# Optimization experiments

Measured on AMD Instinct MI355X. Metric: run time of the kernel, lower is better.

Reference implementation:

```python
import jax, jax.numpy as jnp
import numpy as np

D = 768       # input_dim / model width
H = 3072      # expert hidden width (init arg 'output_dim')
E = 8         # num_experts
K = 2         # top_k
NOISE_STD = 0.1
B, S = 2, 1024


def setup_inputs() -> dict:
    key = jax.random.key(0)
    ks = jax.random.split(key, 16)
    sd = lambda fan_in: 1.0 / np.sqrt(fan_in)
    return {
        "x": jax.random.normal(ks[0], (B, S, D), dtype=jnp.float32),
        "noise": jax.random.normal(ks[1], (B, S, E), dtype=jnp.float32),
        # router
        "Wr": jax.random.normal(ks[2], (D, E), dtype=jnp.float32) * sd(D),
        "br": jnp.zeros((E,), dtype=jnp.float32),
        # stacked expert FFNs: d -> h -> d
        "W1": jax.random.normal(ks[3], (E, D, H), dtype=jnp.float32) * sd(D),
        "b1": jnp.zeros((E, H), dtype=jnp.float32),
        "W2": jax.random.normal(ks[4], (E, H, D), dtype=jnp.float32) * sd(H),
        "b2": jnp.zeros((E, D), dtype=jnp.float32),
        # shared expert
        "Ws1": jax.random.normal(ks[5], (D, H), dtype=jnp.float32) * sd(D),
        "bs1": jnp.zeros((H,), dtype=jnp.float32),
        "Ws2": jax.random.normal(ks[6], (H, D), dtype=jnp.float32) * sd(H),
        "bs2": jnp.zeros((D,), dtype=jnp.float32),
        # mixing scalars (alpha trainable, beta frozen in torch)
        "alpha": jnp.float32(0.3),
        "beta": jnp.float32(0.7),
    }


def reference(x, noise, Wr, br, W1, b1, W2, b2, Ws1, bs1, Ws2, bs2, alpha, beta):
    b, s, d = x.shape
    xt = x.reshape(-1, d)                       # [T, D]
    nt = noise.reshape(-1, E)                   # [T, E]
    T = xt.shape[0]

    # router: noisy logits -> top-k -> softmax over selected experts only
    logits = xt @ Wr + br + NOISE_STD * nt      # [T, E]
    top_vals, top_idx = jax.lax.top_k(logits, K)  # [T, K]
    top_w = jax.nn.softmax(top_vals, axis=-1)     # softmax over -inf-masked logits == softmax over top-k
    gates = jnp.zeros((T, E), dtype=x.dtype).at[jnp.arange(T)[:, None], top_idx].set(top_w)  # [T, E], 0 elsewhere

    # experts (dense over E; non-selected contributions are zeroed by gates)
    h = jax.nn.leaky_relu(jnp.einsum('td,edh->teh', xt, W1) + b1, negative_slope=0.01)  # [T, E, H]
    y = jnp.einsum('teh,ehd->ted', h, W2) + b2                                          # [T, E, D]
    moe_out = jnp.einsum('ted,te->td', y, gates)                                        # [T, D]

    # shared expert
    sh = jax.nn.leaky_relu(xt @ Ws1 + bs1, negative_slope=0.01)
    shared_out = sh @ Ws2 + bs2                                                         # [T, D]

    w = jax.nn.softmax(jnp.stack([alpha, beta]))
    out = shared_out * w[0] + moe_out * w[1]
    return out.reshape(b, s, d)
```

## Files before the change

kernel.cpp:

```cpp
#include <hip/hip_runtime.h>
#include <hip/hip_bf16.h>
#include <cstdio>
#include <cstdint>

#define TNUM 2048
#define DDIM 768
#define HDIM 3072
#define ENUM 8

#define WAITVM(N) asm volatile("s_waitcnt vmcnt(" #N ")" ::: "memory")
#define MEMFENCE() asm volatile("" ::: "memory")

typedef __attribute__((ext_vector_type(8))) __bf16 bf16x8;
typedef __attribute__((ext_vector_type(4))) float f32x4;
typedef __attribute__((ext_vector_type(8))) unsigned short ushort8_t;

__device__ __forceinline__ unsigned short f2bf(float f) {
    __bf16 h = (__bf16)f;
    unsigned short u;
    __builtin_memcpy(&u, &h, 2);
    return u;
}

__device__ __forceinline__ void async_cp16(const unsigned short* g, unsigned short* l) {
    __builtin_amdgcn_global_load_lds((const __attribute__((address_space(1))) void*)g,
                                     (__attribute__((address_space(3))) void*)l,
                                     16, 0, 0);
}

__global__ void cast_x_kernel(const float* __restrict__ x, unsigned short* __restrict__ xb) {
    int i = (blockIdx.x * 256 + threadIdx.x) * 8;
    float4 a = *(const float4*)(x + i);
    float4 b = *(const float4*)(x + i + 4);
    ushort4 lo = make_ushort4(f2bf(a.x), f2bf(a.y), f2bf(a.z), f2bf(a.w));
    ushort4 hi = make_ushort4(f2bf(b.x), f2bf(b.y), f2bf(b.z), f2bf(b.w));
    *(ushort4*)(xb + i) = lo;
    *(ushort4*)(xb + i + 4) = hi;
}

__global__ __launch_bounds__(256)
void transw_kernel(const float* __restrict__ W1, const float* __restrict__ W2,
                   const float* __restrict__ Ws1, const float* __restrict__ Ws2,
                   unsigned short* __restrict__ W1t, unsigned short* __restrict__ W2t,
                   unsigned short* __restrict__ Ws1t, unsigned short* __restrict__ Ws2t) {
    int z = blockIdx.z;
    const float* in; unsigned short* out; int R, C;
    if (z < 8)       { in = W1 + (size_t)z * DDIM * HDIM; out = W1t + (size_t)z * HDIM * DDIM; R = DDIM; C = HDIM; }
    else if (z < 16) { int e = z - 8; in = W2 + (size_t)e * HDIM * DDIM; out = W2t + (size_t)e * DDIM * HDIM; R = HDIM; C = DDIM; }
    else if (z == 16){ in = Ws1; out = Ws1t; R = DDIM; C = HDIM; }
    else             { in = Ws2; out = Ws2t; R = HDIM; C = DDIM; }
    int nx = C / 128;
    int c0 = (blockIdx.x % nx) * 128, r0 = (blockIdx.x / nx) * 128;
    __shared__ __align__(16) unsigned int tileT32[128 * 68];
    int tid = threadIdx.x;
    int l15 = tid & 15;
    int g = tid >> 4;
    int par = (g >> 1) & 1;
    int hf = g & 1;
    int cb = hf * 64 + l15 * 4;
    #pragma unroll
    for (int p = 0; p < 16; p++) {
        int unit = p * 16 + g;
        int r = unit >> 1;
        float4 v = *(const float4*)(in + (size_t)(r0 + r) * C + c0 + cb);
        unsigned int m01 = (unsigned int)f2bf(v.x) | ((unsigned int)f2bf(v.y) << 16);
        unsigned int m23 = (unsigned int)f2bf(v.z) | ((unsigned int)f2bf(v.w) << 16);
        unsigned int o01 = __shfl_xor(m01, 32);
        unsigned int o23 = __shfl_xor(m23, 32);
        unsigned int wA = par ? ((o23 & 0xffffu) | (m23 << 16))
                              : ((m01 & 0xffffu) | (o01 << 16));
        unsigned int wB = par ? ((o23 >> 16) | (m23 & 0xffff0000u))
                              : ((m01 >> 16) | (o01 & 0xffff0000u));
        int ca = cb + par * 2;
        int rp = unit >> 2;
        int cq = ca >> 2;
        int woff = 4 * (((rp >> 2) + 3 * cq) & 15) + (((rp & 3) + cq) & 3);
        tileT32[ca * 68 + woff] = wA;
        tileT32[(ca + 1) * 68 + woff] = wB;
    }
    __syncthreads();
    #pragma unroll
    for (int p = 0; p < 8; p++) {
        int cc = p * 16 + g;
        int cqp = cc >> 2;
        const uint4 W = *(const uint4*)&tileT32[cc * 68 + 4 * ((l15 + 3 * cqp) & 15)];
        unsigned int a0 = W.x, a1 = W.y, a2 = W.z, a3 = W.w;
        int rsel = cqp & 3;
        if (rsel & 1) { unsigned int t = a0; a0 = a1; a1 = a2; a2 = a3; a3 = t; }
        if (rsel & 2) { unsigned int t0 = a0, t1 = a1; a0 = a2; a1 = a3; a2 = t0; a3 = t1; }
        uint4 ov; ov.x = a0; ov.y = a1; ov.z = a2; ov.w = a3;
        *(uint4*)(out + (size_t)(c0 + cc) * R + r0 + l15 * 8) = ov;
    }
}

__global__ void router_kernel(const float* __restrict__ x, const float* __restrict__ noise,
                              const float* __restrict__ Wr, const float* __restrict__ br,
                              int* __restrict__ counts, int* __restrict__ list,
                              int* __restrict__ inv, float* __restrict__ tokp) {
    int lane = threadIdx.x & 63;
    int t = blockIdx.x * 4 + (threadIdx.x >> 6);
    float acc[8];
    #pragma unroll
    for (int e = 0; e < 8; e++) acc[e] = 0.f;
    #pragma unroll
    for (int i = 0; i < 12; i++) {
        int d = i * 64 + lane;
        float xv = x[t * DDIM + d];
        float4 w0 = *(const float4*)(Wr + d * 8);
        float4 w1 = *(const float4*)(Wr + d * 8 + 4);
        acc[0] += xv * w0.x; acc[1] += xv * w0.y; acc[2] += xv * w0.z; acc[3] += xv * w0.w;
        acc[4] += xv * w1.x; acc[5] += xv * w1.y; acc[6] += xv * w1.z; acc[7] += xv * w1.w;
    }
    #pragma unroll
    for (int e = 0; e < 8; e++) {
        #pragma unroll
        for (int off2 = 32; off2 >= 1; off2 >>= 1)
            acc[e] += __shfl_xor(acc[e], off2, 64);
    }
    if (lane == 0) {
        float lg[8];
        #pragma unroll
        for (int e = 0; e < 8; e++) lg[e] = acc[e] + br[e] + 0.1f * noise[t * 8 + e];
        int e0 = 0;
        #pragma unroll
        for (int e = 1; e < 8; e++) if (lg[e] > lg[e0]) e0 = e;
        int e1 = -1;
        #pragma unroll
        for (int e = 0; e < 8; e++) if (e != e0 && (e1 < 0 || lg[e] > lg[e1])) e1 = e;
        float m = fmaxf(lg[e0], lg[e1]);
        float p0 = expf(lg[e0] - m), p1 = expf(lg[e1] - m);
        float inv_s = 1.f / (p0 + p1);
        int s0 = atomicAdd(&counts[e0], 1);
        list[e0 * TNUM + s0] = t;
        int s1 = atomicAdd(&counts[e1], 1);
        list[e1 * TNUM + s1] = t;
        inv[t * 2 + 0] = (e0 << 16) | s0;
        inv[t * 2 + 1] = (e1 << 16) | s1;
        tokp[t * 2 + 0] = p0 * inv_s;
        tokp[t * 2 + 1] = p1 * inv_s;
    }
}

__global__ void finalize_kernel(const int* __restrict__ counts, int* __restrict__ offs,
                                const float* __restrict__ alpha, const float* __restrict__ beta,
                                float* __restrict__ scal) {
    int s = 0;
    for (int e = 0; e < 8; e++) { offs[e] = s; s += counts[e]; }
    offs[8] = s;
    float a = alpha[0], b = beta[0];
    float m = fmaxf(a, b);
    float ea = expf(a - m), eb = expf(b - m);
    float inv = 1.f / (ea + eb);
    scal[0] = ea * inv;
    scal[1] = eb * inv;
}


__global__ __launch_bounds__(256, 3)
void ffn1_kernel(const unsigned short* __restrict__ xb,
                 const unsigned short* __restrict__ W1t,
                 const unsigned short* __restrict__ Ws1t,
                 const float* __restrict__ b1, const float* __restrict__ bs1,
                 const int* __restrict__ counts, const int* __restrict__ offs,
                 const int* __restrict__ list,
                 unsigned short* __restrict__ hbuf) {
    int j = blockIdx.z * 8 + blockIdx.x;
    int y = blockIdx.y;
    int mt0 = y / 12, ntl = y % 12;
    int cnt, hbase, n0, mbase, ntiles;
    const unsigned short* Bmat;
    const float* bias;
    const int* lst = nullptr;
    if (j < 16) {
        int e = j >> 1, nh = j & 1;
        cnt = counts[e];
        ntiles = (cnt + 127) >> 7;
        mbase = 0;
        hbase = offs[e];
        n0 = nh * 1536 + ntl * 128;
        Bmat = W1t + (size_t)e * HDIM * DDIM;
        bias = b1 + e * HDIM;
        lst = list + e * TNUM;
    } else {
        int q = j - 16;
        int ms = q >> 1, nh = q & 1;
        mbase = ms * 512;
        ntiles = 4;
        cnt = 1 << 30;
        hbase = 2 * TNUM;
        n0 = nh * 1536 + ntl * 128;
        Bmat = Ws1t;
        bias = bs1;
    }
    if (mt0 >= ntiles) return;

    __shared__ __align__(16) unsigned short As[3][512 * 8];
    __shared__ __align__(16) unsigned short Bs[3][512 * 8];

    int tid = threadIdx.x;
    int w = tid >> 6, lane = tid & 63;
    int l15 = lane & 15, quad = lane >> 4;
    int wm = (w & 1) * 64, wn = (w >> 1) * 64;

    const unsigned short* gB[2];
    int ldsoff[2];
    int rowl[2];
    #pragma unroll
    for (int r = 0; r < 2; r++) {
        int rc = r * 4 + w;
        rowl[r] = rc * 16 + l15;
        gB[r] = Bmat + (size_t)(n0 + rowl[r]) * DDIM + quad * 8;
        ldsoff[r] = rc * 512;
    }
    int rcA = (w & 1) * 4;
    int rcB = (w >> 1) * 4;
    const int KT = DDIM / 32;

    for (int mt = mt0; mt < ntiles; mt += 4) {
        int m0 = mbase + mt * 128;
        const unsigned short* gA[2];
        #pragma unroll
        for (int r = 0; r < 2; r++) {
            int row;
            if (lst) row = lst[min(m0 + rowl[r], cnt - 1)];
            else     row = m0 + rowl[r];
            gA[r] = xb + (size_t)row * DDIM + quad * 8;
        }

        f32x4 zero = {0.f, 0.f, 0.f, 0.f};
        f32x4 acc[4][4];
        #pragma unroll
        for (int i = 0; i < 4; i++)
            #pragma unroll
            for (int jj = 0; jj < 4; jj++) acc[i][jj] = zero;

        __builtin_amdgcn_s_barrier();
        MEMFENCE();
        #pragma unroll
        for (int t = 0; t < 2; t++)
            #pragma unroll
            for (int r = 0; r < 2; r++) {
                async_cp16(gA[r] + t * 32, &As[t][ldsoff[r]]);
                async_cp16(gB[r] + t * 32, &Bs[t][ldsoff[r]]);
            }

        #pragma unroll 1
        for (int kt = 0; kt < KT; kt++) {
            if (kt == KT - 1) { WAITVM(0); } else { WAITVM(4); }
            __builtin_amdgcn_s_barrier();
            MEMFENCE();
            int cur = kt % 3;
            if (kt + 2 < KT) {
                int nb = (kt + 2) % 3;
                int ko = (kt + 2) * 32;
                #pragma unroll
                for (int r = 0; r < 2; r++) {
                    async_cp16(gA[r] + ko, &As[nb][ldsoff[r]]);
                    async_cp16(gB[r] + ko, &Bs[nb][ldsoff[r]]);
                }
            }
            bf16x8 af[4], bv[4];
            #pragma unroll
            for (int i = 0; i < 4; i++)
                af[i] = *(const bf16x8*)&As[cur][((rcA + i) * 64 + quad * 16 + l15) * 8];
            #pragma unroll
            for (int jj = 0; jj < 4; jj++)
                bv[jj] = *(const bf16x8*)&Bs[cur][((rcB + jj) * 64 + quad * 16 + l15) * 8];
            #pragma unroll
            for (int i = 0; i < 4; i++)
                #pragma unroll
                for (int jj = 0; jj < 4; jj++)
                    acc[i][jj] = __builtin_amdgcn_mfma_f32_16x16x32_bf16(af[i], bv[jj], acc[i][jj], 0, 0, 0);
        }

        #pragma unroll
        for (int i = 0; i < 4; i++) {
            int rbase = m0 + wm + i * 16 + quad * 4;
            #pragma unroll
            for (int jj = 0; jj < 4; jj++) {
                int gc = n0 + wn + jj * 16 + l15;
                float bvl = bias[gc];
                #pragma unroll
                for (int r = 0; r < 4; r++) {
                    int gr = rbase + r;
                    if (gr < cnt) {
                        float v = acc[i][jj][r] + bvl;
                        v = v > 0.f ? v : 0.01f * v;
                        hbuf[(size_t)(hbase + gr) * HDIM + gc] = f2bf(v);
                    }
                }
            }
        }
    }
}

__global__ __launch_bounds__(256, 4)
void ffn2_kernel(const unsigned short* __restrict__ hbuf,
                 const unsigned short* __restrict__ W2t,
                 const unsigned short* __restrict__ Ws2t,
                 const int* __restrict__ counts, const int* __restrict__ offs,
                 float* __restrict__ ybuf) {
    int j = blockIdx.z * 8 + blockIdx.x;
    int y = blockIdx.y;
    int mt0 = y / 6, ntl = y % 6;
    int cnt, hbase, mbase, kh, ntiles;
    const unsigned short* Bmat;
    if (j < 16) {
        int e = j >> 1; kh = j & 1;
        cnt = counts[e];
        ntiles = (cnt + 63) >> 6;
        mbase = 0;
        hbase = offs[e];
        Bmat = W2t + (size_t)e * DDIM * HDIM;
    } else {
        int q = j - 16;
        int mh = q >> 1; kh = q & 1;
        mbase = mh * 512;
        ntiles = 8;
        cnt = 1 << 30;
        hbase = 2 * TNUM;
        Bmat = Ws2t;
    }
    if (mt0 >= ntiles) return;
    int n0 = ntl * 128;
    int kbase = kh * (HDIM / 2);

    __shared__ __align__(16) unsigned short As[3][256 * 8];
    __shared__ __align__(16) unsigned short Bs[3][512 * 8];

    int tid = threadIdx.x;
    int w = tid >> 6, lane = tid & 63;
    int l15 = lane & 15, quad = lane >> 4;
    int wm = (w & 1) * 32, wn = (w >> 1) * 64;

    const unsigned short* gB[2];
    int ldsoffB[2];
    #pragma unroll
    for (int r = 0; r < 2; r++) {
        int rc = r * 4 + w;
        gB[r] = Bmat + (size_t)(n0 + rc * 16 + l15) * HDIM + kbase + quad * 8;
        ldsoffB[r] = rc * 512;
    }
    int rcA = (w & 1) * 2;
    int rcB = (w >> 1) * 4;
    const int KT = (HDIM / 2) / 32;
    int rowl = w * 16 + l15;
    float* yb = ybuf + (size_t)kh * 6144 * DDIM;

    for (int mt = mt0; mt < ntiles; mt += 8) {
        int m0 = mbase + mt * 64;
        int ra = (j < 16) ? min(m0 + rowl, cnt - 1) : (m0 + rowl);
        const unsigned short* gA0 = hbuf + (size_t)(hbase + ra) * HDIM + kbase + quad * 8;

        f32x4 zero = {0.f, 0.f, 0.f, 0.f};
        f32x4 acc[2][4];
        #pragma unroll
        for (int i = 0; i < 2; i++)
            #pragma unroll
            for (int jj = 0; jj < 4; jj++) acc[i][jj] = zero;

        __builtin_amdgcn_s_barrier();
        MEMFENCE();
        #pragma unroll
        for (int t = 0; t < 2; t++) {
            async_cp16(gA0 + t * 32, &As[t][w * 512]);
            #pragma unroll
            for (int r = 0; r < 2; r++) async_cp16(gB[r] + t * 32, &Bs[t][ldsoffB[r]]);
        }

        #pragma unroll 1
        for (int kt = 0; kt < KT; kt++) {
            if (kt == KT - 1) { WAITVM(0); } else { WAITVM(3); }
            __builtin_amdgcn_s_barrier();
            MEMFENCE();
            int cur = kt % 3;
            if (kt + 2 < KT) {
                int nb = (kt + 2) % 3;
                int ko = (kt + 2) * 32;
                async_cp16(gA0 + ko, &As[nb][w * 512]);
                #pragma unroll
                for (int r = 0; r < 2; r++) async_cp16(gB[r] + ko, &Bs[nb][ldsoffB[r]]);
            }
            bf16x8 af[2], bv[4];
            #pragma unroll
            for (int i = 0; i < 2; i++)
                af[i] = *(const bf16x8*)&As[cur][((rcA + i) * 64 + quad * 16 + l15) * 8];
            #pragma unroll
            for (int jj = 0; jj < 4; jj++)
                bv[jj] = *(const bf16x8*)&Bs[cur][((rcB + jj) * 64 + quad * 16 + l15) * 8];
            #pragma unroll
            for (int i = 0; i < 2; i++)
                #pragma unroll
                for (int jj = 0; jj < 4; jj++)
                    acc[i][jj] = __builtin_amdgcn_mfma_f32_16x16x32_bf16(af[i], bv[jj], acc[i][jj], 0, 0, 0);
        }

        #pragma unroll
        for (int i = 0; i < 2; i++) {
            int rbase = m0 + wm + i * 16 + quad * 4;
            #pragma unroll
            for (int r = 0; r < 4; r++) {
                int gr = rbase + r;
                if (gr >= cnt) continue;
                float* orow = yb + (size_t)(hbase + gr) * DDIM + n0 + wn;
                #pragma unroll
                for (int jj = 0; jj < 4; jj++)
                    orow[jj * 16 + l15] = acc[i][jj][r];
            }
        }
    }
}

__global__ void mix_kernel(const float* __restrict__ ybuf, const int* __restrict__ inv,
                           const float* __restrict__ tokp, const int* __restrict__ offs,
                           const float* __restrict__ b2, const float* __restrict__ bs2,
                           const float* __restrict__ scal, float* __restrict__ out) {
    int t = blockIdx.x;
    int c = threadIdx.x * 4;
    int i0 = inv[t * 2 + 0], i1 = inv[t * 2 + 1];
    int e0 = i0 >> 16, sl0 = i0 & 0xFFFF;
    int e1 = i1 >> 16, sl1 = i1 & 0xFFFF;
    float p0 = tokp[t * 2 + 0], p1 = tokp[t * 2 + 1];
    float ws = scal[0], wmx = scal[1];
    size_t rA = (size_t)(offs[e0] + sl0) * DDIM + c;
    size_t rB = (size_t)(offs[e1] + sl1) * DDIM + c;
    size_t rS = (size_t)(2 * TNUM + t) * DDIM + c;
    const float* y0 = ybuf;
    const float* y1 = ybuf + (size_t)6144 * DDIM;
    float4 vA0 = *(const float4*)(y0 + rA);
    float4 vA1 = *(const float4*)(y1 + rA);
    float4 vB0 = *(const float4*)(y0 + rB);
    float4 vB1 = *(const float4*)(y1 + rB);
    float4 vS0 = *(const float4*)(y0 + rS);
    float4 vS1 = *(const float4*)(y1 + rS);
    float4 bA = *(const float4*)(b2 + e0 * DDIM + c);
    float4 bB = *(const float4*)(b2 + e1 * DDIM + c);
    float4 bS = *(const float4*)(bs2 + c);
    float4 o;
    o.x = ws * (vS0.x + vS1.x + bS.x) + wmx * (p0 * (vA0.x + vA1.x + bA.x) + p1 * (vB0.x + vB1.x + bB.x));
    o.y = ws * (vS0.y + vS1.y + bS.y) + wmx * (p0 * (vA0.y + vA1.y + bA.y) + p1 * (vB0.y + vB1.y + bB.y));
    o.z = ws * (vS0.z + vS1.z + bS.z) + wmx * (p0 * (vA0.z + vA1.z + bA.z) + p1 * (vB0.z + vB1.z + bB.z));
    o.w = ws * (vS0.w + vS1.w + bS.w) + wmx * (p0 * (vA0.w + vA1.w + bA.w) + p1 * (vB0.w + vB1.w + bB.w));
    *(float4*)(out + (size_t)t * DDIM + c) = o;
}

extern "C" void kernel_launch(void* const* d_in, const int* in_sizes, int n_in,
                              void* d_out, int out_size, void* d_ws, size_t ws_size,
                              hipStream_t stream) {
    const float* x     = (const float*)d_in[0];
    const float* noise = (const float*)d_in[1];
    const float* Wr    = (const float*)d_in[2];
    const float* br    = (const float*)d_in[3];
    const float* W1    = (const float*)d_in[4];
    const float* b1    = (const float*)d_in[5];
    const float* W2    = (const float*)d_in[6];
    const float* b2    = (const float*)d_in[7];
    const float* Ws1   = (const float*)d_in[8];
    const float* bs1   = (const float*)d_in[9];
    const float* Ws2   = (const float*)d_in[10];
    const float* bs2   = (const float*)d_in[11];
    const float* alpha = (const float*)d_in[12];
    const float* beta  = (const float*)d_in[13];

    char* ws = (char*)d_ws;
    size_t off = 0;
    auto alloc = [&](size_t bytes) -> char* {
        char* p = ws + off;
        off = (off + bytes + 255) & ~(size_t)255;
        return p;
    };
    int*   counts = (int*)  alloc(ENUM * 4);
    int*   offs   = (int*)  alloc(16 * 4);
    float* scal   = (float*)alloc(2 * 4);
    int*   list   = (int*)  alloc((size_t)ENUM * TNUM * 4);
    int*   inv    = (int*)  alloc((size_t)TNUM * 2 * 4);
    float* tokp   = (float*)alloc((size_t)TNUM * 2 * 4);
    unsigned short* xb   = (unsigned short*)alloc((size_t)TNUM * DDIM * 2);
    unsigned short* W1t  = (unsigned short*)alloc((size_t)ENUM * HDIM * DDIM * 2);
    unsigned short* Ws1t = (unsigned short*)alloc((size_t)HDIM * DDIM * 2);
    unsigned short* W2t  = (unsigned short*)alloc((size_t)ENUM * DDIM * HDIM * 2);
    unsigned short* Ws2t = (unsigned short*)alloc((size_t)DDIM * HDIM * 2);
    unsigned short* hbuf = (unsigned short*)alloc((size_t)(3 * TNUM) * HDIM * 2);
    float* ybuf = (float*)W1t;
    if (off > ws_size) {
        fprintf(stderr, "kernel_launch: workspace too small (need %zu, have %zu)\n", off, ws_size);
        return;
    }

    hipMemsetAsync(counts, 0, ENUM * 4, stream);

    cast_x_kernel<<<dim3((TNUM * DDIM / 8) / 256), dim3(256), 0, stream>>>(x, xb);
    transw_kernel<<<dim3(144, 1, 18), dim3(256), 0, stream>>>(W1, W2, Ws1, Ws2, W1t, W2t, Ws1t, Ws2t);
    router_kernel<<<dim3(TNUM / 4), dim3(256), 0, stream>>>(x, noise, Wr, br, counts, list, inv, tokp);
    finalize_kernel<<<dim3(1), dim3(1), 0, stream>>>(counts, offs, alpha, beta, scal);
    ffn1_kernel<<<dim3(8, 48, 3), dim3(256), 0, stream>>>(xb, W1t, Ws1t, b1, bs1, counts, offs, list, hbuf);
    ffn2_kernel<<<dim3(8, 48, 3), dim3(256), 0, stream>>>(hbuf, W2t, Ws2t, counts, offs, ybuf);
    mix_kernel<<<dim3(TNUM), dim3(192), 0, stream>>>(ybuf, inv, tokp, offs, b2, bs2, scal, (float*)d_out);
}
```

Before: 462.3 us.

## Merge prep kernels, overlap W2 transpose with FFN1, drop FFN2 split-K

Cast, W1/Ws1 transpose and the router now run in one combined pre-kernel. The W2/Ws2 transpose moves into extra blocks of the FFN1 launch so it overlaps the first GEMM, and the finalize kernel goes away because each kernel recomputes prefix offsets and mixing weights locally. FFN2 no longer splits K across two halves, which removes the second ybuf partial and its extra reads in mix. In exchange, FFN2 has fewer parallel blocks with longer K loops, and FFN1 shares its LDS layout with the transpose path.

After: 506.7 us. 9.6% more time.

```diff
diff --git a/kernel.cpp b/kernel.cpp
--- a/kernel.cpp
+++ b/kernel.cpp
@@ -13,7 +13,6 @@
 
 typedef __attribute__((ext_vector_type(8))) __bf16 bf16x8;
 typedef __attribute__((ext_vector_type(4))) float f32x4;
-typedef __attribute__((ext_vector_type(8))) unsigned short ushort8_t;
 
 __device__ __forceinline__ unsigned short f2bf(float f) {
     __bf16 h = (__bf16)f;
@@ -28,30 +27,10 @@
                                      16, 0, 0);
 }
 
-__global__ void cast_x_kernel(const float* __restrict__ x, unsigned short* __restrict__ xb) {
-    int i = (blockIdx.x * 256 + threadIdx.x) * 8;
-    float4 a = *(const float4*)(x + i);
-    float4 b = *(const float4*)(x + i + 4);
-    ushort4 lo = make_ushort4(f2bf(a.x), f2bf(a.y), f2bf(a.z), f2bf(a.w));
-    ushort4 hi = make_ushort4(f2bf(b.x), f2bf(b.y), f2bf(b.z), f2bf(b.w));
-    *(ushort4*)(xb + i) = lo;
-    *(ushort4*)(xb + i + 4) = hi;
-}
-
-__global__ __launch_bounds__(256)
-void transw_kernel(const float* __restrict__ W1, const float* __restrict__ W2,
-                   const float* __restrict__ Ws1, const float* __restrict__ Ws2,
-                   unsigned short* __restrict__ W1t, unsigned short* __restrict__ W2t,
-                   unsigned short* __restrict__ Ws1t, unsigned short* __restrict__ Ws2t) {
-    int z = blockIdx.z;
-    const float* in; unsigned short* out; int R, C;
-    if (z < 8)       { in = W1 + (size_t)z * DDIM * HDIM; out = W1t + (size_t)z * HDIM * DDIM; R = DDIM; C = HDIM; }
-    else if (z < 16) { int e = z - 8; in = W2 + (size_t)e * HDIM * DDIM; out = W2t + (size_t)e * DDIM * HDIM; R = HDIM; C = DDIM; }
-    else if (z == 16){ in = Ws1; out = Ws1t; R = DDIM; C = HDIM; }
-    else             { in = Ws2; out = Ws2t; R = HDIM; C = DDIM; }
-    int nx = C / 128;
-    int c0 = (blockIdx.x % nx) * 128, r0 = (blockIdx.x / nx) * 128;
-    __shared__ __align__(16) unsigned int tileT32[128 * 68];
+__device__ __forceinline__ void transpose_tile(const float* __restrict__ in,
+                                               unsigned short* __restrict__ out,
+                                               int R, int C, int c0, int r0,
+                                               unsigned int* tileT32) {
     int tid = threadIdx.x;
     int l15 = tid & 15;
     int g = tid >> 4;
@@ -93,12 +72,35 @@
     }
 }
 
-__global__ void router_kernel(const float* __restrict__ x, const float* __restrict__ noise,
-                              const float* __restrict__ Wr, const float* __restrict__ br,
-                              int* __restrict__ counts, int* __restrict__ list,
-                              int* __restrict__ inv, float* __restrict__ tokp) {
+__global__ __launch_bounds__(256)
+void pre_kernel(const float* __restrict__ x, const float* __restrict__ noise,
+                const float* __restrict__ Wr, const float* __restrict__ br,
+                const float* __restrict__ W1, const float* __restrict__ Ws1,
+                unsigned short* __restrict__ W1t, unsigned short* __restrict__ Ws1t,
+                unsigned short* __restrict__ xb,
+                int* __restrict__ counts, int* __restrict__ list,
+                int* __restrict__ inv, float* __restrict__ tokp) {
+    __shared__ __align__(16) unsigned int tileT32[128 * 68];
+    int b = blockIdx.x;
+    if (b < 1296) {
+        int m = b / 144, t = b % 144;
+        const float* in       = (m < 8) ? (W1 + (size_t)m * DDIM * HDIM) : Ws1;
+        unsigned short* out   = (m < 8) ? (W1t + (size_t)m * HDIM * DDIM) : Ws1t;
+        transpose_tile(in, out, DDIM, HDIM, (t % 24) * 128, (t / 24) * 128, tileT32);
+        return;
+    }
+    if (b < 2064) {
+        int i = ((b - 1296) * 256 + threadIdx.x) * 8;
+        float4 a = *(const float4*)(x + i);
+        float4 bb = *(const float4*)(x + i + 4);
+        ushort4 lo = make_ushort4(f2bf(a.x), f2bf(a.y), f2bf(a.z), f2bf(a.w));
+        ushort4 hi = make_ushort4(f2bf(bb.x), f2bf(bb.y), f2bf(bb.z), f2bf(bb.w));
+        *(ushort4*)(xb + i) = lo;
+        *(ushort4*)(xb + i + 4) = hi;
+        return;
+    }
     int lane = threadIdx.x & 63;
-    int t = blockIdx.x * 4 + (threadIdx.x >> 6);
+    int t = (b - 2064) * 4 + (threadIdx.x >> 6);
     float acc[8];
     #pragma unroll
     for (int e = 0; e < 8; e++) acc[e] = 0.f;
@@ -141,32 +143,39 @@
     }
 }
 
-__global__ void finalize_kernel(const int* __restrict__ counts, int* __restrict__ offs,
-                                const float* __restrict__ alpha, const float* __restrict__ beta,
-                                float* __restrict__ scal) {
-    int s = 0;
-    for (int e = 0; e < 8; e++) { offs[e] = s; s += counts[e]; }
-    offs[8] = s;
-    float a = alpha[0], b = beta[0];
-    float m = fmaxf(a, b);
-    float ea = expf(a - m), eb = expf(b - m);
-    float inv = 1.f / (ea + eb);
-    scal[0] = ea * inv;
-    scal[1] = eb * inv;
-}
-
-
 __global__ __launch_bounds__(256, 3)
 void ffn1_kernel(const unsigned short* __restrict__ xb,
                  const unsigned short* __restrict__ W1t,
                  const unsigned short* __restrict__ Ws1t,
                  const float* __restrict__ b1, const float* __restrict__ bs1,
-                 const int* __restrict__ counts, const int* __restrict__ offs,
-                 const int* __restrict__ list,
-                 unsigned short* __restrict__ hbuf) {
+                 const int* __restrict__ counts, const int* __restrict__ list,
+                 unsigned short* __restrict__ hbuf,
+                 const float* __restrict__ W2, const float* __restrict__ Ws2,
+                 unsigned short* __restrict__ W2t, unsigned short* __restrict__ Ws2t) {
+    __shared__ __align__(16) unsigned char smem[49152];
+
+    if (blockIdx.z >= 3) {
+        int q = (blockIdx.z - 3) * 384 + blockIdx.y * 8 + blockIdx.x;
+        if (q >= 1296) return;
+        int m = q / 144, t = q % 144;
+        const float* in     = (m < 8) ? (W2 + (size_t)m * HDIM * DDIM) : Ws2;
+        unsigned short* out = (m < 8) ? (W2t + (size_t)m * DDIM * HDIM) : Ws2t;
+        transpose_tile(in, out, HDIM, DDIM, (t % 6) * 128, (t / 6) * 128, (unsigned int*)smem);
+        return;
+    }
+
+    unsigned short* As = (unsigned short*)smem;
+    unsigned short* Bs = (unsigned short*)(smem + 24576);
+
     int j = blockIdx.z * 8 + blockIdx.x;
     int y = blockIdx.y;
     int mt0 = y / 12, ntl = y % 12;
+
+    int offv[8];
+    { int s = 0;
+      #pragma unroll
+      for (int e = 0; e < 8; e++) { offv[e] = s; s += counts[e]; } }
+
     int cnt, hbase, n0, mbase, ntiles;
     const unsigned short* Bmat;
     const float* bias;
@@ -176,7 +185,7 @@
         cnt = counts[e];
         ntiles = (cnt + 127) >> 7;
         mbase = 0;
-        hbase = offs[e];
+        hbase = offv[e];
         n0 = nh * 1536 + ntl * 128;
         Bmat = W1t + (size_t)e * HDIM * DDIM;
         bias = b1 + e * HDIM;
@@ -194,27 +203,23 @@
     }
     if (mt0 >= ntiles) return;
 
-    __shared__ __align__(16) unsigned short As[3][512 * 8];
-    __shared__ __align__(16) unsigned short Bs[3][512 * 8];
-
     int tid = threadIdx.x;
     int w = tid >> 6, lane = tid & 63;
     int l15 = lane & 15, quad = lane >> 4;
     int wm = (w & 1) * 64, wn = (w >> 1) * 64;
+    int rcA = (w & 1) * 4;
+    int rcB = (w >> 1) * 4;
+    const int KT = DDIM / 32;
 
     const unsigned short* gB[2];
-    int ldsoff[2];
-    int rowl[2];
+    int ldsoff[2], rowl[2];
     #pragma unroll
     for (int r = 0; r < 2; r++) {
         int rc = r * 4 + w;
         rowl[r] = rc * 16 + l15;
+        ldsoff[r] = rc * 512;
         gB[r] = Bmat + (size_t)(n0 + rowl[r]) * DDIM + quad * 8;
-        ldsoff[r] = rc * 512;
-    }
-    int rcA = (w & 1) * 4;
-    int rcB = (w >> 1) * 4;
-    const int KT = DDIM / 32;
+    }
 
     for (int mt = mt0; mt < ntiles; mt += 4) {
         int m0 = mbase + mt * 128;
@@ -240,8 +245,8 @@
         for (int t = 0; t < 2; t++)
             #pragma unroll
             for (int r = 0; r < 2; r++) {
-                async_cp16(gA[r] + t * 32, &As[t][ldsoff[r]]);
-                async_cp16(gB[r] + t * 32, &Bs[t][ldsoff[r]]);
+                async_cp16(gA[r] + t * 32, As + t * 4096 + ldsoff[r]);
+                async_cp16(gB[r] + t * 32, Bs + t * 4096 + ldsoff[r]);
             }
 
         #pragma unroll 1
@@ -255,17 +260,17 @@
                 int ko = (kt + 2) * 32;
                 #pragma unroll
                 for (int r = 0; r < 2; r++) {
-                    async_cp16(gA[r] + ko, &As[nb][ldsoff[r]]);
-                    async_cp16(gB[r] + ko, &Bs[nb][ldsoff[r]]);
+                    async_cp16(gA[r] + ko, As + nb * 4096 + ldsoff[r]);
+                    async_cp16(gB[r] + ko, Bs + nb * 4096 + ldsoff[r]);
                 }
             }
             bf16x8 af[4], bv[4];
             #pragma unroll
             for (int i = 0; i < 4; i++)
-                af[i] = *(const bf16x8*)&As[cur][((rcA + i) * 64 + quad * 16 + l15) * 8];
+                af[i] = *(const bf16x8*)(As + cur * 4096 + ((rcA + i) * 64 + quad * 16 + l15) * 8);
             #pragma unroll
             for (int jj = 0; jj < 4; jj++)
-                bv[jj] = *(const bf16x8*)&Bs[cur][((rcB + jj) * 64 + quad * 16 + l15) * 8];
+                bv[jj] = *(const bf16x8*)(Bs + cur * 4096 + ((rcB + jj) * 64 + quad * 16 + l15) * 8);
             #pragma unroll
             for (int i = 0; i < 4; i++)
                 #pragma unroll
@@ -298,59 +303,62 @@
 void ffn2_kernel(const unsigned short* __restrict__ hbuf,
                  const unsigned short* __restrict__ W2t,
                  const unsigned short* __restrict__ Ws2t,
-                 const int* __restrict__ counts, const int* __restrict__ offs,
+                 const int* __restrict__ counts,
                  float* __restrict__ ybuf) {
+    __shared__ __align__(16) unsigned short As[3][256 * 8];
+    __shared__ __align__(16) unsigned short Bs[3][512 * 8];
+
     int j = blockIdx.z * 8 + blockIdx.x;
     int y = blockIdx.y;
     int mt0 = y / 6, ntl = y % 6;
-    int cnt, hbase, mbase, kh, ntiles;
+    int n0 = ntl * 128;
+
+    int offv[8];
+    { int s = 0;
+      #pragma unroll
+      for (int e = 0; e < 8; e++) { offv[e] = s; s += counts[e]; } }
+
+    int cnt, hbase, mbase, ntiles;
     const unsigned short* Bmat;
-    if (j < 16) {
-        int e = j >> 1; kh = j & 1;
+    if (j < 8) {
+        int e = j;
         cnt = counts[e];
         ntiles = (cnt + 63) >> 6;
         mbase = 0;
-        hbase = offs[e];
+        hbase = offv[e];
         Bmat = W2t + (size_t)e * DDIM * HDIM;
     } else {
-        int q = j - 16;
-        int mh = q >> 1; kh = q & 1;
-        mbase = mh * 512;
-        ntiles = 8;
+        int s = j - 8;
+        mbase = s * 256;
+        ntiles = 4;
         cnt = 1 << 30;
         hbase = 2 * TNUM;
         Bmat = Ws2t;
     }
     if (mt0 >= ntiles) return;
-    int n0 = ntl * 128;
-    int kbase = kh * (HDIM / 2);
-
-    __shared__ __align__(16) unsigned short As[3][256 * 8];
-    __shared__ __align__(16) unsigned short Bs[3][512 * 8];
 
     int tid = threadIdx.x;
     int w = tid >> 6, lane = tid & 63;
     int l15 = lane & 15, quad = lane >> 4;
     int wm = (w & 1) * 32, wn = (w >> 1) * 64;
+    int rcA = (w & 1) * 2;
+    int rcB = (w >> 1) * 4;
+    const int KT = HDIM / 32;
+    int rowl = w * 16 + l15;
 
     const unsigned short* gB[2];
     int ldsoffB[2];
     #pragma unroll
     for (int r = 0; r < 2; r++) {
         int rc = r * 4 + w;
-        gB[r] = Bmat + (size_t)(n0 + rc * 16 + l15) * HDIM + kbase + quad * 8;
+        gB[r] = Bmat + (size_t)(n0 + rc * 16 + l15) * HDIM + quad * 8;
         ldsoffB[r] = rc * 512;
     }
-    int rcA = (w & 1) * 2;
-    int rcB = (w >> 1) * 4;
-    const int KT = (HDIM / 2) / 32;
-    int rowl = w * 16 + l15;
-    float* yb = ybuf + (size_t)kh * 6144 * DDIM;
 
     for (int mt = mt0; mt < ntiles; mt += 8) {
         int m0 = mbase + mt * 64;
-        int ra = (j < 16) ? min(m0 + rowl, cnt - 1) : (m0 + rowl);
-        const unsigned short* gA0 = hbuf + (size_t)(hbase + ra) * HDIM + kbase + quad * 8;
+        int ra = (j < 8) ? min(m0 + rowl, cnt - 1) : (m0 + rowl);
+        const unsigned short* gA0 = hbuf + (size_t)(hbase + ra) * HDIM + quad * 8;
 
         f32x4 zero = {0.f, 0.f, 0.f, 0.f};
         f32x4 acc[2][4];
@@ -402,7 +410,7 @@
             for (int r = 0; r < 4; r++) {
                 int gr = rbase + r;
                 if (gr >= cnt) continue;
-                float* orow = yb + (size_t)(hbase + gr) * DDIM + n0 + wn;
+                float* orow = ybuf + (size_t)(hbase + gr) * DDIM + n0 + wn;
                 #pragma unroll
                 for (int jj = 0; jj < 4; jj++)
                     orow[jj * 16 + l15] = acc[i][jj][r];
@@ -412,35 +420,40 @@
 }
 
 __global__ void mix_kernel(const float* __restrict__ ybuf, const int* __restrict__ inv,
-                           const float* __restrict__ tokp, const int* __restrict__ offs,
+                           const float* __restrict__ tokp, const int* __restrict__ counts,
                            const float* __restrict__ b2, const float* __restrict__ bs2,
-                           const float* __restrict__ scal, float* __restrict__ out) {
+                           const float* __restrict__ alpha, const float* __restrict__ beta,
+                           float* __restrict__ out) {
     int t = blockIdx.x;
     int c = threadIdx.x * 4;
+    int offv[8];
+    { int s = 0;
+      #pragma unroll
+      for (int e = 0; e < 8; e++) { offv[e] = s; s += counts[e]; } }
+    float a = alpha[0], bsc = beta[0];
+    float m = fmaxf(a, bsc);
+    float ea = expf(a - m), eb = expf(bsc - m);
+    float is = 1.f / (ea + eb);
+    float ws = ea * is, wmx = eb * is;
+
     int i0 = inv[t * 2 + 0], i1 = inv[t * 2 + 1];
     int e0 = i0 >> 16, sl0 = i0 & 0xFFFF;
     int e1 = i1 >> 16, sl1 = i1 & 0xFFFF;
     float p0 = tokp[t * 2 + 0], p1 = tokp[t * 2 + 1];
-    float ws = scal[0], wmx = scal[1];
-    size_t rA = (size_t)(offs[e0] + sl0) * DDIM + c;
-    size_t rB = (size_t)(offs[e1] + sl1) * DDIM + c;
+    size_t rA = (size_t)(offv[e0] + sl0) * DDIM + c;
+    size_t rB = (size_t)(offv[e1] + sl1) * DDIM + c;
     size_t rS = (size_t)(2 * TNUM + t) * DDIM + c;
-    const float* y0 = ybuf;
-    const float* y1 = ybuf + (size_t)6144 * DDIM;
-    float4 vA0 = *(const float4*)(y0 + rA);
-    float4 vA1 = *(const float4*)(y1 + rA);
-    float4 vB0 = *(const float4*)(y0 + rB);
-    float4 vB1 = *(const float4*)(y1 + rB);
-    float4 vS0 = *(const float4*)(y0 + rS);
-    float4 vS1 = *(const float4*)(y1 + rS);
+    float4 vA = *(const float4*)(ybuf + rA);
+    float4 vB = *(const float4*)(ybuf + rB);
+    float4 vS = *(const float4*)(ybuf + rS);
     float4 bA = *(const float4*)(b2 + e0 * DDIM + c);
     float4 bB = *(const float4*)(b2 + e1 * DDIM + c);
     float4 bS = *(const float4*)(bs2 + c);
     float4 o;
-    o.x = ws * (vS0.x + vS1.x + bS.x) + wmx * (p0 * (vA0.x + vA1.x + bA.x) + p1 * (vB0.x + vB1.x + bB.x));
-    o.y = ws * (vS0.y + vS1.y + bS.y) + wmx * (p0 * (vA0.y + vA1.y + bA.y) + p1 * (vB0.y + vB1.y + bB.y));
-    o.z = ws * (vS0.z + vS1.z + bS.z) + wmx * (p0 * (vA0.z + vA1.z + bA.z) + p1 * (vB0.z + vB1.z + bB.z));
-    o.w = ws * (vS0.w + vS1.w + bS.w) + wmx * (p0 * (vA0.w + vA1.w + bA.w) + p1 * (vB0.w + vB1.w + bB.w));
+    o.x = ws * (vS.x + bS.x) + wmx * (p0 * (vA.x + bA.x) + p1 * (vB.x + bB.x));
+    o.y = ws * (vS.y + bS.y) + wmx * (p0 * (vA.y + bA.y) + p1 * (vB.y + bB.y));
+    o.z = ws * (vS.z + bS.z) + wmx * (p0 * (vA.z + bA.z) + p1 * (vB.z + bB.z));
+    o.w = ws * (vS.w + bS.w) + wmx * (p0 * (vA.w + bA.w) + p1 * (vB.w + bB.w));
     *(float4*)(out + (size_t)t * DDIM + c) = o;
 }
 
@@ -470,8 +483,6 @@
         return p;
     };
     int*   counts = (int*)  alloc(ENUM * 4);
-    int*   offs   = (int*)  alloc(16 * 4);
-    float* scal   = (float*)alloc(2 * 4);
     int*   list   = (int*)  alloc((size_t)ENUM * TNUM * 4);
     int*   inv    = (int*)  alloc((size_t)TNUM * 2 * 4);
     float* tokp   = (float*)alloc((size_t)TNUM * 2 * 4);
@@ -489,11 +500,11 @@
 
     hipMemsetAsync(counts, 0, ENUM * 4, stream);
 
-    cast_x_kernel<<<dim3((TNUM * DDIM / 8) / 256), dim3(256), 0, stream>>>(x, xb);
-    transw_kernel<<<dim3(144, 1, 18), dim3(256), 0, stream>>>(W1, W2, Ws1, Ws2, W1t, W2t, Ws1t, Ws2t);
-    router_kernel<<<dim3(TNUM / 4), dim3(256), 0, stream>>>(x, noise, Wr, br, counts, list, inv, tokp);
-    finalize_kernel<<<dim3(1), dim3(1), 0, stream>>>(counts, offs, alpha, beta, scal);
-    ffn1_kernel<<<dim3(8, 48, 3), dim3(256), 0, stream>>>(xb, W1t, Ws1t, b1, bs1, counts, offs, list, hbuf);
-    ffn2_kernel<<<dim3(8, 48, 3), dim3(256), 0, stream>>>(hbuf, W2t, Ws2t, counts, offs, ybuf);
-    mix_kernel<<<dim3(TNUM), dim3(192), 0, stream>>>(ybuf, inv, tokp, offs, b2, bs2, scal, (float*)d_out);
-}
+    pre_kernel<<<dim3(2576), dim3(256), 0, stream>>>(x, noise, Wr, br, W1, Ws1,
+                                                     W1t, Ws1t, xb, counts, list, inv, tokp);
+    ffn1_kernel<<<dim3(8, 48, 7), dim3(256), 0, stream>>>(xb, W1t, Ws1t, b1, bs1, counts, list,
+                                                          hbuf, W2, Ws2, W2t, Ws2t);
+    ffn2_kernel<<<dim3(8, 48, 2), dim3(256), 0, stream>>>(hbuf, W2t, Ws2t, counts, ybuf);
+    mix_kernel<<<dim3(TNUM), dim3(192), 0, stream>>>(ybuf, inv, tokp, counts, b2, bs2,
+                                                     alpha, beta, (float*)d_out);
+}
```
